# Performance work log

Hardware: AMD Instinct MI355X
Metric: run time of the kernel (lower is better)

## Reference

```python
import jax, jax.numpy as jnp
import numpy as np

BS, GRID, A, CH = 32, 2704, 3, 85   # 52x52 YOLO grid, 3 anchors, 80 classes + 5
HW = 52
VDIM, H, SEL = 1024, 512, 32
EPS = 1e-8


def setup_inputs() -> dict:
    key = jax.random.key(0)
    ks = jax.random.split(key, 16)
    s = 0.02
    return {
        "boxes": jax.random.uniform(ks[0], (BS, GRID, A, CH), dtype=jnp.float32),
        "x_feat": jax.random.normal(ks[1], (BS, VDIM, HW, HW), dtype=jnp.float32),
        "tag_emb": jax.random.normal(ks[2], (BS, SEL, H), dtype=jnp.float32),
        "pos_emb": jax.random.normal(ks[3], (BS, SEL, H), dtype=jnp.float32),
        "lang": jax.random.normal(ks[4], (BS, H), dtype=jnp.float32),
        "W_vs": jax.random.normal(ks[5], (VDIM, H), dtype=jnp.float32) * s,
        "b_vs": jnp.zeros((H,), jnp.float32),
        "W_ts": jax.random.normal(ks[6], (H, H), dtype=jnp.float32) * s,
        "b_ts": jnp.zeros((H,), jnp.float32),
        "W_vs_pos": jax.random.normal(ks[7], (H, H), dtype=jnp.float32) * s,
        "b_vs_pos": jnp.zeros((H,), jnp.float32),
        "W_tag": jax.random.normal(ks[8], (H, H), dtype=jnp.float32) * s,
        "b_tag": jnp.zeros((H,), jnp.float32),
        "W_soft": jax.random.normal(ks[9], (H, 2), dtype=jnp.float32) * s,
        "b_soft": jnp.zeros((2,), jnp.float32),
    }


def reference(boxes, x_feat, tag_emb, pos_emb, lang,
              W_vs, b_vs, W_ts, b_ts, W_vs_pos, b_vs_pos,
              W_tag, b_tag, W_soft, b_soft):
    bs = boxes.shape[0]
    # --- topk grid selection on mean objectness (channel 4) ---
    score = jnp.mean(boxes, axis=2)[:, :, 4]                     # [bs, grid]
    _, idx = jax.lax.top_k(score, SEL)                           # [bs, SEL]
    # torch's scatter->masked_select recovers selected grids in ascending
    # index order (not topk-value order), so sort the indices.
    idx = jnp.sort(idx, axis=1)
    # gather selected boxes: [bs, SEL, A, CH]
    boxes_sel = jnp.take_along_axis(boxes, idx[:, :, None, None], axis=1)
    # gather selected visual features: [bs, SEL, VDIM]
    feat = x_feat.reshape(bs, VDIM, -1).transpose(0, 2, 1)       # [bs, grid, VDIM]
    i_sel = jnp.take_along_axis(feat, idx[:, :, None], axis=1)
    # --- gated multimodal fusion ---
    vis = i_sel @ W_vs + b_vs                                    # [bs, SEL, H]
    lang_e = (lang @ W_ts + b_ts)[:, None, :]                    # [bs, 1, H]
    logits = ((vis + tag_emb + pos_emb) @ W_soft + b_soft) / 0.03
    w = jax.nn.log_softmax(logits, axis=-1)                      # [bs, SEL, 2]
    vis2 = ((vis * w[..., 0:1]) @ W_vs_pos + b_vs_pos
            + (tag_emb * w[..., 1:2]) @ W_tag + b_tag
            + pos_emb)                                           # [bs, SEL, H]
    # --- head (eval): cosine similarity vs language, top-1 grid mask ---
    vn = vis2 / (jnp.linalg.norm(vis2, axis=-1, keepdims=True) + EPS)
    ln = lang_e / (jnp.linalg.norm(lang_e, axis=-1, keepdims=True) + EPS)
    sim = jnp.sum(vn * ln, axis=-1)                              # [bs, SEL]
    top_grid = jnp.argmax(sim, axis=1)                           # [bs]
    # --- get_boxes: gather top grid, xywh->xyxy, top-1 box by objectness ---
    sel = jnp.take_along_axis(boxes_sel, top_grid[:, None, None, None], axis=1)
    sel = jax.lax.stop_gradient(sel[:, 0])                       # [bs, A, CH] (.data in torch)
    x1 = sel[..., 0] - sel[..., 2] / 2
    y1 = sel[..., 1] - sel[..., 3] / 2
    x2 = x1 + sel[..., 2]
    y2 = y1 + sel[..., 3]
    bxyxy = jnp.concatenate(
        [jnp.stack([x1, y1, x2, y2], axis=-1), sel[..., 4:]], axis=-1)
    j = jnp.argmax(bxyxy[:, :, 4], axis=1)                       # [bs]
    box_pred = jnp.take_along_axis(bxyxy[:, :, :5], j[:, None, None], axis=1)
    return box_pred, sim
```

## Files before the change

### kernel.cpp

```cpp
#include <hip/hip_runtime.h>
#include <hip/hip_bf16.h>
#include <math.h>

#define BS   32
#define GRID_N 2704
#define A_N  3
#define CH   85
#define VDIM 1024
#define HDIM 512
#define SEL  32
#define ROWS (BS*SEL)

#define WS_ISEL   1024
#define WS_VIS    (WS_ISEL + ROWS*VDIM)
#define WS_VIS2   (WS_VIS + ROWS*HDIM)
#define WS_SCORE  (WS_VIS2 + ROWS*HDIM)
#define WS_W01    (WS_SCORE + BS*GRID_N)
#define WS_TOTAL_FLOATS (WS_W01 + ROWS*2)

__global__ __launch_bounds__(256) void score_kernel(const float* __restrict__ boxes,
                                                    float* __restrict__ score) {
    int t = blockIdx.x * 256 + threadIdx.x;
    const float* p = boxes + (long)t * (A_N * CH);
    score[t] = (p[4] + p[CH + 4] + p[2 * CH + 4]) * (1.0f / 3.0f);
}

__global__ __launch_bounds__(256) void topk_kernel(const float* __restrict__ score,
                                                   int* __restrict__ idx_out) {
    __shared__ float sc[GRID_N];
    __shared__ float cv[256];
    __shared__ int   ci[256];
    __shared__ int   selg[SEL];
    __shared__ float rbv[4];
    __shared__ int   rbi[4];
    int b = blockIdx.x, tid = threadIdx.x;
    for (int g = tid; g < GRID_N; g += 256) sc[g] = score[b * GRID_N + g];
    __syncthreads();
    {
        float bv = -3.4e38f; int bi = 0x7fffffff;
        for (int g = tid; g < GRID_N; g += 256) {
            float v = sc[g];
            if (v > bv || (v == bv && g < bi)) { bv = v; bi = g; }
        }
        cv[tid] = bv; ci[tid] = bi;
    }
    __syncthreads();
    for (int i = 0; i < SEL; ++i) {
        float bv = cv[tid]; int bi = ci[tid];
        for (int off = 32; off; off >>= 1) {
            float ov = __shfl_down(bv, off);
            int   oi = __shfl_down(bi, off);
            if (ov > bv || (ov == bv && oi < bi)) { bv = ov; bi = oi; }
        }
        int lane = tid & 63, wid = tid >> 6;
        if (lane == 0) { rbv[wid] = bv; rbi[wid] = bi; }
        __syncthreads();
        if (tid == 0) {
            float fv = rbv[0]; int fi = rbi[0];
            for (int w = 1; w < 4; ++w)
                if (rbv[w] > fv || (rbv[w] == fv && rbi[w] < fi)) { fv = rbv[w]; fi = rbi[w]; }
            selg[i] = fi;
            sc[fi] = -3.4e38f;
        }
        __syncthreads();
        if (ci[tid] == selg[i]) {
            float nv = -3.4e38f; int ni = 0x7fffffff;
            for (int g = tid; g < GRID_N; g += 256) {
                float v = sc[g];
                if (v > nv || (v == nv && g < ni)) { nv = v; ni = g; }
            }
            cv[tid] = nv; ci[tid] = ni;
        }
        __syncthreads();
    }
    if (tid < SEL) {
        int my = selg[tid], rank = 0;
        for (int j = 0; j < SEL; ++j) rank += (selg[j] < my);
        idx_out[b * SEL + rank] = my;
    }
}

__global__ __launch_bounds__(256) void gather_kernel(const float* __restrict__ xf,
                                                     const int* __restrict__ idx,
                                                     float* __restrict__ isel) {
    int r = blockIdx.x;
    int b = r >> 5;
    int g = idx[r];
    const float* src = xf + (long)b * VDIM * GRID_N + g;
    float* dst = isel + (long)r * VDIM;
    #pragma unroll
    for (int j = 0; j < 4; ++j) {
        int v = threadIdx.x + j * 256;
        dst[v] = src[(long)v * GRID_N];
    }
}

__global__ __launch_bounds__(256) void w01_kernel(const float* __restrict__ vis,
                                                  const float* __restrict__ tag,
                                                  const float* __restrict__ pos,
                                                  const float* __restrict__ Wsoft,
                                                  const float* __restrict__ bsoft,
                                                  float* __restrict__ w01) {
    int tid = threadIdx.x;
    int lane = tid & 63;
    int r = blockIdx.x * 4 + (tid >> 6);
    int k0 = lane * 8;
    const float* vr = vis + (long)r * HDIM + k0;
    const float* tr = tag + (long)r * HDIM + k0;
    const float* pr = pos + (long)r * HDIM + k0;
    const float* wr = Wsoft + 2 * k0;
    float s0 = 0.f, s1 = 0.f;
    #pragma unroll
    for (int j = 0; j < 2; ++j) {
        float4 v = *(const float4*)&vr[j * 4];
        float4 t = *(const float4*)&tr[j * 4];
        float4 p = *(const float4*)&pr[j * 4];
        float4 wA = *(const float4*)&wr[j * 8];
        float4 wB = *(const float4*)&wr[j * 8 + 4];
        float e0 = v.x + t.x + p.x, e1 = v.y + t.y + p.y;
        float e2 = v.z + t.z + p.z, e3 = v.w + t.w + p.w;
        s0 += e0 * wA.x + e1 * wA.z + e2 * wB.x + e3 * wB.z;
        s1 += e0 * wA.y + e1 * wA.w + e2 * wB.y + e3 * wB.w;
    }
    #pragma unroll
    for (int off = 32; off; off >>= 1) {
        s0 += __shfl_down(s0, off);
        s1 += __shfl_down(s1, off);
    }
    if (lane == 0) {
        float l0 = (s0 + bsoft[0]) * (1.0f / 0.03f);
        float l1 = (s1 + bsoft[1]) * (1.0f / 0.03f);
        float m = fmaxf(l0, l1);
        float lse = m + logf(expf(l0 - m) + expf(l1 - m));
        *(float2*)&w01[r * 2] = make_float2(l0 - lse, l1 - lse);
    }
}

#define KT 32
#define WIDX(k, gi) (((k) * 64) + (((gi) ^ ((k) & 7)) << 2))

__global__ __launch_bounds__(512) void gemm1_kernel(const float* __restrict__ A,
                                                    const float* __restrict__ W,
                                                    const float* __restrict__ bias,
                                                    float* __restrict__ out) {
    __shared__ float As[2][2][KT][34];
    __shared__ float Ws[2][2][KT * 64];
    __shared__ float Rs[32][68];
    int tid = threadIdx.x;
    int g = tid >> 8;
    int tg = tid & 255;
    int bx = blockIdx.x, by = blockIdx.y;
    int ct = tg & 15, rt = tg >> 4;
    int c0 = by * 64 + ct * 4;
    int srow = tg >> 3;
    int sk4  = (tg & 7) * 4;
    int wk = tg >> 3;
    int wg0 = (tg & 7) * 2;
    const long kbase = (long)g * 512;
    const float* arow = A + (long)(bx * 32 + srow) * VDIM + kbase;
    const float* wbase = W + kbase * HDIM + by * 64;
    float* wsg = &Ws[g][0][0];

    float acc[2][4] = {{0.f,0.f,0.f,0.f},{0.f,0.f,0.f,0.f}};
    {
        float4 a0  = *(const float4*)&arow[sk4];
        float4 w0v = *(const float4*)&wbase[(long)wk * HDIM + wg0 * 4];
        float4 w1v = *(const float4*)&wbase[(long)wk * HDIM + wg0 * 4 + 4];
        As[g][0][sk4 + 0][srow] = a0.x; As[g][0][sk4 + 1][srow] = a0.y;
        As[g][0][sk4 + 2][srow] = a0.z; As[g][0][sk4 + 3][srow] = a0.w;
        *(float4*)&wsg[WIDX(wk, wg0)]     = w0v;
        *(float4*)&wsg[WIDX(wk, wg0 + 1)] = w1v;
    }
    __syncthreads();
    for (int t = 0; t < 16; ++t) {
        int buf = t & 1;
        float4 na, nw0, nw1;
        if (t < 15) {
            na  = *(const float4*)&arow[(t + 1) * KT + sk4];
            nw0 = *(const float4*)&wbase[(long)((t + 1) * KT + wk) * HDIM + wg0 * 4];
            nw1 = *(const float4*)&wbase[(long)((t + 1) * KT + wk) * HDIM + wg0 * 4 + 4];
        }
        const float* wsb = &Ws[g][buf][0];
        #pragma unroll
        for (int k = 0; k < KT; ++k) {
            float4 w = *(const float4*)&wsb[WIDX(k, ct)];
            float2 a = *(const float2*)&As[g][buf][k][rt * 2];
            acc[0][0] += a.x * w.x; acc[0][1] += a.x * w.y;
            acc[0][2] += a.x * w.z; acc[0][3] += a.x * w.w;
            acc[1][0] += a.y * w.x; acc[1][1] += a.y * w.y;
            acc[1][2] += a.y * w.z; acc[1][3] += a.y * w.w;
        }
        if (t < 15) {
            float* wsn = &Ws[g][buf ^ 1][0];
            As[g][buf ^ 1][sk4 + 0][srow] = na.x; As[g][buf ^ 1][sk4 + 1][srow] = na.y;
            As[g][buf ^ 1][sk4 + 2][srow] = na.z; As[g][buf ^ 1][sk4 + 3][srow] = na.w;
            *(float4*)&wsn[WIDX(wk, wg0)]     = nw0;
            *(float4*)&wsn[WIDX(wk, wg0 + 1)] = nw1;
        }
        __syncthreads();
    }
    if (g == 1) {
        *(float4*)&Rs[rt * 2 + 0][ct * 4] = make_float4(acc[0][0], acc[0][1], acc[0][2], acc[0][3]);
        *(float4*)&Rs[rt * 2 + 1][ct * 4] = make_float4(acc[1][0], acc[1][1], acc[1][2], acc[1][3]);
    }
    __syncthreads();
    if (g == 0) {
        float4 bv = *(const float4*)&bias[c0];
        #pragma unroll
        for (int i = 0; i < 2; ++i) {
            float4 r = *(const float4*)&Rs[rt * 2 + i][ct * 4];
            float4 o;
            o.x = acc[i][0] + r.x + bv.x; o.y = acc[i][1] + r.y + bv.y;
            o.z = acc[i][2] + r.z + bv.z; o.w = acc[i][3] + r.w + bv.w;
            *(float4*)&out[(long)(bx * 32 + rt * 2 + i) * HDIM + c0] = o;
        }
    }
}

__global__ __launch_bounds__(512) void gemm2_kernel(const float* __restrict__ vis,
                                                    const float* __restrict__ tag,
                                                    const float* __restrict__ pos,
                                                    const float* __restrict__ w01,
                                                    const float* __restrict__ Wvp,
                                                    const float* __restrict__ Wtag,
                                                    const float* __restrict__ bvp,
                                                    const float* __restrict__ btag,
                                                    float* __restrict__ out) {
    __shared__ float As[2][2][KT][34];
    __shared__ float Ws[2][2][KT * 64];
    __shared__ float Rs[32][68];
    int tid = threadIdx.x;
    int g = tid >> 8;
    int tg = tid & 255;
    int bx = blockIdx.x, by = blockIdx.y;
    int ct = tg & 15, rt = tg >> 4;
    int c0 = by * 64 + ct * 4;
    int srow = tg >> 3;
    int sk4  = (tg & 7) * 4;
    int wk = tg >> 3;
    int wg0 = (tg & 7) * 2;
    int grow = bx * 32 + srow;
    float2 wv = *(const float2*)&w01[grow * 2];
    float scale = g ? wv.y : wv.x;
    const float* arow = (g ? tag : vis) + (long)grow * HDIM;
    const float* wbase = (g ? Wtag : Wvp) + by * 64;
    float* wsg = &Ws[g][0][0];

    float acc[2][4] = {{0.f,0.f,0.f,0.f},{0.f,0.f,0.f,0.f}};
    {
        float4 a0  = *(const float4*)&arow[sk4];
        float4 w0v = *(const float4*)&wbase[(long)wk * HDIM + wg0 * 4];
        float4 w1v = *(const float4*)&wbase[(long)wk * HDIM + wg0 * 4 + 4];
        As[g][0][sk4 + 0][srow] = a0.x * scale; As[g][0][sk4 + 1][srow] = a0.y * scale;
        As[g][0][sk4 + 2][srow] = a0.z * scale; As[g][0][sk4 + 3][srow] = a0.w * scale;
        *(float4*)&wsg[WIDX(wk, wg0)]     = w0v;
        *(float4*)&wsg[WIDX(wk, wg0 + 1)] = w1v;
    }
    __syncthreads();
    for (int t = 0; t < 16; ++t) {
        int buf = t & 1;
        float4 na, nw0, nw1;
        if (t < 15) {
            na  = *(const float4*)&arow[(t + 1) * KT + sk4];
            nw0 = *(const float4*)&wbase[(long)((t + 1) * KT + wk) * HDIM + wg0 * 4];
            nw1 = *(const float4*)&wbase[(long)((t + 1) * KT + wk) * HDIM + wg0 * 4 + 4];
        }
        const float* wsb = &Ws[g][buf][0];
        #pragma unroll
        for (int k = 0; k < KT; ++k) {
            float4 w = *(const float4*)&wsb[WIDX(k, ct)];
            float2 a = *(const float2*)&As[g][buf][k][rt * 2];
            acc[0][0] += a.x * w.x; acc[0][1] += a.x * w.y;
            acc[0][2] += a.x * w.z; acc[0][3] += a.x * w.w;
            acc[1][0] += a.y * w.x; acc[1][1] += a.y * w.y;
            acc[1][2] += a.y * w.z; acc[1][3] += a.y * w.w;
        }
        if (t < 15) {
            float* wsn = &Ws[g][buf ^ 1][0];
            As[g][buf ^ 1][sk4 + 0][srow] = na.x * scale; As[g][buf ^ 1][sk4 + 1][srow] = na.y * scale;
            As[g][buf ^ 1][sk4 + 2][srow] = na.z * scale; As[g][buf ^ 1][sk4 + 3][srow] = na.w * scale;
            *(float4*)&wsn[WIDX(wk, wg0)]     = nw0;
            *(float4*)&wsn[WIDX(wk, wg0 + 1)] = nw1;
        }
        __syncthreads();
    }
    if (g == 1) {
        *(float4*)&Rs[rt * 2 + 0][ct * 4] = make_float4(acc[0][0], acc[0][1], acc[0][2], acc[0][3]);
        *(float4*)&Rs[rt * 2 + 1][ct * 4] = make_float4(acc[1][0], acc[1][1], acc[1][2], acc[1][3]);
    }
    __syncthreads();
    if (g == 0) {
        float4 b1 = *(const float4*)&bvp[c0];
        float4 b2 = *(const float4*)&btag[c0];
        #pragma unroll
        for (int i = 0; i < 2; ++i) {
            int r = bx * 32 + rt * 2 + i;
            float4 rr = *(const float4*)&Rs[rt * 2 + i][ct * 4];
            float4 p = *(const float4*)&pos[(long)r * HDIM + c0];
            float4 o;
            o.x = acc[i][0] + rr.x + b1.x + b2.x + p.x;
            o.y = acc[i][1] + rr.y + b1.y + b2.y + p.y;
            o.z = acc[i][2] + rr.z + b1.z + b2.z + p.z;
            o.w = acc[i][3] + rr.w + b1.w + b2.w + p.w;
            *(float4*)&out[(long)r * HDIM + c0] = o;
        }
    }
}

__global__ __launch_bounds__(256) void final_kernel(const float* __restrict__ vis2,
                                                    const float* __restrict__ lang,
                                                    const float* __restrict__ Wts,
                                                    const float* __restrict__ bts,
                                                    const int* __restrict__ idx,
                                                    const float* __restrict__ boxes,
                                                    float* __restrict__ out) {
    __shared__ float ll[HDIM];
    __shared__ float lns[HDIM];
    __shared__ float red[4];
    __shared__ float sims[SEL];
    int b = blockIdx.x, tid = threadIdx.x;
    int lane = tid & 63, wid = tid >> 6;
    ll[tid]       = lang[b * HDIM + tid];
    ll[tid + 256] = lang[b * HDIM + tid + 256];
    __syncthreads();
    for (int h = tid; h < HDIM; h += 256) {
        float a0 = 0.f, a1 = 0.f, a2 = 0.f, a3 = 0.f;
        for (int k = 0; k < HDIM; k += 4) {
            a0 += ll[k + 0] * Wts[(long)(k + 0) * HDIM + h];
            a1 += ll[k + 1] * Wts[(long)(k + 1) * HDIM + h];
            a2 += ll[k + 2] * Wts[(long)(k + 2) * HDIM + h];
            a3 += ll[k + 3] * Wts[(long)(k + 3) * HDIM + h];
        }
        lns[h] = ((a0 + a1) + (a2 + a3)) + bts[h];
    }
    __syncthreads();
    float s = lns[tid] * lns[tid] + lns[tid + 256] * lns[tid + 256];
    for (int off = 32; off; off >>= 1) s += __shfl_down(s, off);
    if (lane == 0) red[wid] = s;
    __syncthreads();
    float sscale;
    {
        float t = red[0] + red[1] + red[2] + red[3];
        sscale = 1.0f / (sqrtf(t) + 1e-8f);
    }
    for (int j = 0; j < 8; ++j) {
        int sl = wid + j * 4;
        const float* vr = vis2 + (long)(b * SEL + sl) * HDIM;
        int k = lane * 8;
        float ss = 0.f, dot = 0.f;
        #pragma unroll
        for (int t = 0; t < 8; ++t) {
            float v = vr[k + t];
            ss += v * v;
            dot += v * lns[k + t];
        }
        for (int off = 32; off; off >>= 1) {
            ss += __shfl_down(ss, off);
            dot += __shfl_down(dot, off);
        }
        if (lane == 0) {
            float sim = dot * sscale / (sqrtf(ss) + 1e-8f);
            out[BS * 5 + b * SEL + sl] = sim;
            sims[sl] = sim;
        }
    }
    __syncthreads();
    if (tid == 0) {
        int bsi = 0; float bvv = sims[0];
        for (int sl = 1; sl < SEL; ++sl)
            if (sims[sl] > bvv) { bvv = sims[sl]; bsi = sl; }
        int g = idx[b * SEL + bsi];
        const float* bb = boxes + ((long)(b * GRID_N + g)) * A_N * CH;
        float o0 = bb[4], o1 = bb[CH + 4], o2 = bb[2 * CH + 4];
        int j = 0; float ov = o0;
        if (o1 > ov) { ov = o1; j = 1; }
        if (o2 > ov) { ov = o2; j = 2; }
        const float* sb = bb + j * CH;
        float x = sb[0], y = sb[1], w = sb[2], h = sb[3];
        float x1 = x - w * 0.5f, y1 = y - h * 0.5f;
        out[b * 5 + 0] = x1;
        out[b * 5 + 1] = y1;
        out[b * 5 + 2] = x1 + w;
        out[b * 5 + 3] = y1 + h;
        out[b * 5 + 4] = sb[4];
    }
}

extern "C" void kernel_launch(void* const* d_in, const int* in_sizes, int n_in,
                              void* d_out, int out_size, void* d_ws, size_t ws_size,
                              hipStream_t stream) {
    const float* boxes    = (const float*)d_in[0];
    const float* x_feat   = (const float*)d_in[1];
    const float* tag_emb  = (const float*)d_in[2];
    const float* pos_emb  = (const float*)d_in[3];
    const float* lang     = (const float*)d_in[4];
    const float* W_vs     = (const float*)d_in[5];
    const float* b_vs     = (const float*)d_in[6];
    const float* W_ts     = (const float*)d_in[7];
    const float* b_ts     = (const float*)d_in[8];
    const float* W_vs_pos = (const float*)d_in[9];
    const float* b_vs_pos = (const float*)d_in[10];
    const float* W_tag    = (const float*)d_in[11];
    const float* b_tag    = (const float*)d_in[12];
    const float* W_soft   = (const float*)d_in[13];
    const float* b_soft   = (const float*)d_in[14];
    float* out = (float*)d_out;

    if (ws_size < (size_t)WS_TOTAL_FLOATS * sizeof(float)) return;

    float* wsf   = (float*)d_ws;
    int*   wsidx = (int*)d_ws;
    float* isel  = wsf + WS_ISEL;
    float* vis   = wsf + WS_VIS;
    float* vis2  = wsf + WS_VIS2;
    float* score = wsf + WS_SCORE;
    float* w01   = wsf + WS_W01;

    score_kernel<<<(BS * GRID_N) / 256, 256, 0, stream>>>(boxes, score);
    topk_kernel<<<BS, 256, 0, stream>>>(score, wsidx);
    gather_kernel<<<ROWS, 256, 0, stream>>>(x_feat, wsidx, isel);
    gemm1_kernel<<<dim3(32, 8), 512, 0, stream>>>(isel, W_vs, b_vs, vis);
    w01_kernel<<<ROWS / 4, 256, 0, stream>>>(vis, tag_emb, pos_emb, W_soft, b_soft, w01);
    gemm2_kernel<<<dim3(32, 8), 512, 0, stream>>>(vis, tag_emb, pos_emb, w01,
                                                  W_vs_pos, W_tag, b_vs_pos, b_tag, vis2);
    final_kernel<<<BS, 256, 0, stream>>>(vis2, lang, W_ts, b_ts, wsidx, boxes, out);
}
```

Before: 648.4 us.

## Fuse score computation into topk and softmax gate into gemm2

```diff
diff --git a/kernel.cpp b/kernel.cpp
--- a/kernel.cpp
+++ b/kernel.cpp
@@ -14,18 +14,9 @@
 #define WS_ISEL   1024
 #define WS_VIS    (WS_ISEL + ROWS*VDIM)
 #define WS_VIS2   (WS_VIS + ROWS*HDIM)
-#define WS_SCORE  (WS_VIS2 + ROWS*HDIM)
-#define WS_W01    (WS_SCORE + BS*GRID_N)
-#define WS_TOTAL_FLOATS (WS_W01 + ROWS*2)
-
-__global__ __launch_bounds__(256) void score_kernel(const float* __restrict__ boxes,
-                                                    float* __restrict__ score) {
-    int t = blockIdx.x * 256 + threadIdx.x;
-    const float* p = boxes + (long)t * (A_N * CH);
-    score[t] = (p[4] + p[CH + 4] + p[2 * CH + 4]) * (1.0f / 3.0f);
-}
-
-__global__ __launch_bounds__(256) void topk_kernel(const float* __restrict__ score,
+#define WS_TOTAL_FLOATS (WS_VIS2 + ROWS*HDIM)
+
+__global__ __launch_bounds__(256) void topk_kernel(const float* __restrict__ boxes,
                                                    int* __restrict__ idx_out) {
     __shared__ float sc[GRID_N];
     __shared__ float cv[256];
@@ -34,7 +25,12 @@
     __shared__ float rbv[4];
     __shared__ int   rbi[4];
     int b = blockIdx.x, tid = threadIdx.x;
-    for (int g = tid; g < GRID_N; g += 256) sc[g] = score[b * GRID_N + g];
+    const float* bb = boxes + (long)b * GRID_N * (A_N * CH);
+    for (int g = tid; g < GRID_N; g += 256) {
+        const float* p = bb + (long)g * (A_N * CH);
+        float o0 = p[4], o1 = p[CH + 4], o2 = p[2 * CH + 4];
+        sc[g] = (o0 + o1 + o2) * (1.0f / 3.0f);
+    }
     __syncthreads();
     {
         float bv = -3.4e38f; int bi = 0x7fffffff;
@@ -92,47 +88,6 @@
     for (int j = 0; j < 4; ++j) {
         int v = threadIdx.x + j * 256;
         dst[v] = src[(long)v * GRID_N];
-    }
-}
-
-__global__ __launch_bounds__(256) void w01_kernel(const float* __restrict__ vis,
-                                                  const float* __restrict__ tag,
-                                                  const float* __restrict__ pos,
-                                                  const float* __restrict__ Wsoft,
-                                                  const float* __restrict__ bsoft,
-                                                  float* __restrict__ w01) {
-    int tid = threadIdx.x;
-    int lane = tid & 63;
-    int r = blockIdx.x * 4 + (tid >> 6);
-    int k0 = lane * 8;
-    const float* vr = vis + (long)r * HDIM + k0;
-    const float* tr = tag + (long)r * HDIM + k0;
-    const float* pr = pos + (long)r * HDIM + k0;
-    const float* wr = Wsoft + 2 * k0;
-    float s0 = 0.f, s1 = 0.f;
-    #pragma unroll
-    for (int j = 0; j < 2; ++j) {
-        float4 v = *(const float4*)&vr[j * 4];
-        float4 t = *(const float4*)&tr[j * 4];
-        float4 p = *(const float4*)&pr[j * 4];
-        float4 wA = *(const float4*)&wr[j * 8];
-        float4 wB = *(const float4*)&wr[j * 8 + 4];
-        float e0 = v.x + t.x + p.x, e1 = v.y + t.y + p.y;
-        float e2 = v.z + t.z + p.z, e3 = v.w + t.w + p.w;
-        s0 += e0 * wA.x + e1 * wA.z + e2 * wB.x + e3 * wB.z;
-        s1 += e0 * wA.y + e1 * wA.w + e2 * wB.y + e3 * wB.w;
-    }
-    #pragma unroll
-    for (int off = 32; off; off >>= 1) {
-        s0 += __shfl_down(s0, off);
-        s1 += __shfl_down(s1, off);
-    }
-    if (lane == 0) {
-        float l0 = (s0 + bsoft[0]) * (1.0f / 0.03f);
-        float l1 = (s1 + bsoft[1]) * (1.0f / 0.03f);
-        float m = fmaxf(l0, l1);
-        float lse = m + logf(expf(l0 - m) + expf(l1 - m));
-        *(float2*)&w01[r * 2] = make_float2(l0 - lse, l1 - lse);
     }
 }
 
@@ -220,7 +175,8 @@
 __global__ __launch_bounds__(512) void gemm2_kernel(const float* __restrict__ vis,
                                                     const float* __restrict__ tag,
                                                     const float* __restrict__ pos,
-                                                    const float* __restrict__ w01,
+                                                    const float* __restrict__ Wsoft,
+                                                    const float* __restrict__ bsoft,
                                                     const float* __restrict__ Wvp,
                                                     const float* __restrict__ Wtag,
                                                     const float* __restrict__ bvp,
@@ -229,6 +185,8 @@
     __shared__ float As[2][2][KT][34];
     __shared__ float Ws[2][2][KT * 64];
     __shared__ float Rs[32][68];
+    __shared__ float w0s[2][32];
+    __shared__ float w1s[2][32];
     int tid = threadIdx.x;
     int g = tid >> 8;
     int tg = tid & 255;
@@ -240,17 +198,50 @@
     int wk = tg >> 3;
     int wg0 = (tg & 7) * 2;
     int grow = bx * 32 + srow;
-    float2 wv = *(const float2*)&w01[grow * 2];
-    float scale = g ? wv.y : wv.x;
     const float* arow = (g ? tag : vis) + (long)grow * HDIM;
     const float* wbase = (g ? Wtag : Wvp) + by * 64;
     float* wsg = &Ws[g][0][0];
 
+    float4 a0  = *(const float4*)&arow[sk4];
+    float4 w0v = *(const float4*)&wbase[(long)wk * HDIM + wg0 * 4];
+    float4 w1v = *(const float4*)&wbase[(long)wk * HDIM + wg0 * 4 + 4];
+
+    {
+        int sub = tg & 7;
+        const float* vr = vis + (long)grow * HDIM + sub * 64;
+        const float* tr = tag + (long)grow * HDIM + sub * 64;
+        const float* pr = pos + (long)grow * HDIM + sub * 64;
+        const float* wr = Wsoft + (sub * 64) * 2;
+        float s0 = 0.f, s1 = 0.f;
+        #pragma unroll
+        for (int j = 0; j < 16; ++j) {
+            float4 v = *(const float4*)&vr[j * 4];
+            float4 t = *(const float4*)&tr[j * 4];
+            float4 p = *(const float4*)&pr[j * 4];
+            float4 wA = *(const float4*)&wr[j * 8];
+            float4 wB = *(const float4*)&wr[j * 8 + 4];
+            float e0 = v.x + t.x + p.x, e1 = v.y + t.y + p.y;
+            float e2 = v.z + t.z + p.z, e3 = v.w + t.w + p.w;
+            s0 += e0 * wA.x + e1 * wA.z + e2 * wB.x + e3 * wB.z;
+            s1 += e0 * wA.y + e1 * wA.w + e2 * wB.y + e3 * wB.w;
+        }
+        s0 += __shfl_down(s0, 4, 8); s1 += __shfl_down(s1, 4, 8);
+        s0 += __shfl_down(s0, 2, 8); s1 += __shfl_down(s1, 2, 8);
+        s0 += __shfl_down(s0, 1, 8); s1 += __shfl_down(s1, 1, 8);
+        if (sub == 0) {
+            float l0 = (s0 + bsoft[0]) * (1.0f / 0.03f);
+            float l1 = (s1 + bsoft[1]) * (1.0f / 0.03f);
+            float m = fmaxf(l0, l1);
+            float lse = m + logf(expf(l0 - m) + expf(l1 - m));
+            w0s[g][srow] = l0 - lse;
+            w1s[g][srow] = l1 - lse;
+        }
+    }
+    __syncthreads();
+    float scale = g ? w1s[g][srow] : w0s[g][srow];
+
     float acc[2][4] = {{0.f,0.f,0.f,0.f},{0.f,0.f,0.f,0.f}};
     {
-        float4 a0  = *(const float4*)&arow[sk4];
-        float4 w0v = *(const float4*)&wbase[(long)wk * HDIM + wg0 * 4];
-        float4 w1v = *(const float4*)&wbase[(long)wk * HDIM + wg0 * 4 + 4];
         As[g][0][sk4 + 0][srow] = a0.x * scale; As[g][0][sk4 + 1][srow] = a0.y * scale;
         As[g][0][sk4 + 2][srow] = a0.z * scale; As[g][0][sk4 + 3][srow] = a0.w * scale;
         *(float4*)&wsg[WIDX(wk, wg0)]     = w0v;
@@ -413,15 +404,11 @@
     float* isel  = wsf + WS_ISEL;
     float* vis   = wsf + WS_VIS;
     float* vis2  = wsf + WS_VIS2;
-    float* score = wsf + WS_SCORE;
-    float* w01   = wsf + WS_W01;
-
-    score_kernel<<<(BS * GRID_N) / 256, 256, 0, stream>>>(boxes, score);
-    topk_kernel<<<BS, 256, 0, stream>>>(score, wsidx);
+
+    topk_kernel<<<BS, 256, 0, stream>>>(boxes, wsidx);
     gather_kernel<<<ROWS, 256, 0, stream>>>(x_feat, wsidx, isel);
     gemm1_kernel<<<dim3(32, 8), 512, 0, stream>>>(isel, W_vs, b_vs, vis);
-    w01_kernel<<<ROWS / 4, 256, 0, stream>>>(vis, tag_emb, pos_emb, W_soft, b_soft, w01);
-    gemm2_kernel<<<dim3(32, 8), 512, 0, stream>>>(vis, tag_emb, pos_emb, w01,
+    gemm2_kernel<<<dim3(32, 8), 512, 0, stream>>>(vis, tag_emb, pos_emb, W_soft, b_soft,
                                                   W_vs_pos, W_tag, b_vs_pos, b_tag, vis2);
     final_kernel<<<BS, 256, 0, stream>>>(vis2, lang, W_ts, b_ts, wsidx, boxes, out);
 }
```

Result: slower. 663.9 us (+2.4%).
